# Kernel optimization log

Measured on AMD Instinct MI355X. Metric: run time of the kernel, lower is better.

The kernel has to match this reference:

```python
import jax, jax.numpy as jnp
import numpy as np

N = 512  # n_inputs = n_layers (even)


def setup_inputs() -> dict:
    key = jax.random.key(0)
    ks = jax.random.split(key, 8)
    H = N // 2
    two_pi = 2.0 * np.pi
    return {
        "thetas_full": jax.random.uniform(ks[0], (N, N), jnp.float32, 0.0, two_pi),
        "thetas_inout": jax.random.uniform(ks[1], (2, N), jnp.float32, 0.0, two_pi),
        "pc_losses_full": 0.05 * jax.random.uniform(ks[2], (N, N), jnp.float32),
        "pc_losses_inout": 0.05 * jax.random.uniform(ks[3], (2, N), jnp.float32),
        "mmi_losses_even": 0.05 * jax.random.uniform(ks[4], (N, H), jnp.float32),
        "mmi_losses_odd": 0.05 * jax.random.uniform(ks[5], (N, H - 1), jnp.float32),
        "mmi_imb_even": jax.random.uniform(ks[6], (N, H), jnp.float32, -0.05, 0.05),
        "mmi_imb_odd": jax.random.uniform(ks[7], (N, H - 1), jnp.float32, -0.05, 0.05),
    }


def _pc(M, theta, loss):
    # diag(sqrt(1-loss) * exp(i*theta)) @ M  -- phase shifter on every waveguide
    a = jnp.sqrt(1.0 - loss) * jnp.exp(1j * theta)  # complex64 [n]
    return a[:, None] * M


def _mmi_pairs(top, bot, loss, imb):
    # 2x2 MMI coupler sqrt(1-loss) * [[t, i r], [i r, t]], t=sqrt(.5+imb), r=sqrt(.5-imb)
    a = jnp.sqrt(1.0 - loss)[:, None]
    t = (a * jnp.sqrt(0.5 + imb)[:, None]).astype(top.dtype)
    r = (a * jnp.sqrt(0.5 - imb)[:, None])
    ir = (1j * r).astype(top.dtype)
    return t * top + ir * bot, ir * top + t * bot


def _mmi_even(M, loss, imb):
    # couplers on row pairs (0,1),(2,3),...
    n = M.shape[0]
    P = M.reshape(n // 2, 2, n)
    top, bot = _mmi_pairs(P[:, 0], P[:, 1], loss, imb)
    return jnp.stack([top, bot], axis=1).reshape(n, n)


def _mmi_odd(M, loss, imb):
    # couplers on row pairs (1,2),(3,4),...; rows 0 and n-1 pass through
    n = M.shape[0]
    P = M[1:-1].reshape(n // 2 - 1, 2, n)
    top, bot = _mmi_pairs(P[:, 0], P[:, 1], loss, imb)
    inner = jnp.stack([top, bot], axis=1).reshape(n - 2, n)
    return jnp.concatenate([M[:1], inner, M[-1:]], axis=0)


def _forward(thetas_full, thetas_inout, pc_losses_full, pc_losses_inout,
             mmi_losses_even, mmi_losses_odd, mmi_imb_even, mmi_imb_odd):
    n = thetas_full.shape[1]
    h = n // 2
    M = jnp.eye(n, dtype=jnp.complex64)
    M = _pc(M, thetas_inout[0], pc_losses_inout[0])
    # pack params two layers per scan step (loop body uses indices 2i and 2i+1)
    xs = (thetas_full.reshape(h, 2, n), pc_losses_full.reshape(h, 2, n),
          mmi_losses_even.reshape(h, 2, h), mmi_imb_even.reshape(h, 2, h),
          mmi_losses_odd.reshape(h, 2, h - 1), mmi_imb_odd.reshape(h, 2, h - 1))

    def step(M, x):
        th, lp, le, ie, lo, io = x
        M = _mmi_even(M, le[0], ie[0])
        M = _pc(M, th[0], lp[0])
        M = _mmi_even(M, le[1], ie[1])
        M = _mmi_odd(M, lo[0], io[0])
        M = _pc(M, th[1], lp[1])
        M = _mmi_odd(M, lo[1], io[1])
        return M, None

    M, _ = jax.lax.scan(jax.checkpoint(step), M, xs)
    return _pc(M, thetas_inout[1], pc_losses_inout[1])


def reference(thetas_full, thetas_inout, pc_losses_full, pc_losses_inout,
              mmi_losses_even, mmi_losses_odd, mmi_imb_even, mmi_imb_odd):
    return _forward(thetas_full, thetas_inout, pc_losses_full, pc_losses_inout,
                    mmi_losses_even, mmi_losses_odd, mmi_imb_even, mmi_imb_odd)
```

## Files before the change

### kernel.cpp

```cpp
#include <hip/hip_runtime.h>
#include <math.h>

#define NROWS   512
#define NSTEPS  256
#define PKSTEPS (NSTEPS + 2)

__device__ float4 g_pk[PKSTEPS * 5 * 256];
__device__ float2 g_io[1024];


__device__ __forceinline__ float2 pc_coef(float th, float loss) {
  float a = sqrtf(1.0f - loss);
  float s, c;
  sincosf(th, &s, &c);
  return make_float2(a * c, a * s);
}
__device__ __forceinline__ float2 mmi_coef(float loss, float imb) {
  float a = sqrtf(1.0f - loss);
  return make_float2(a * sqrtf(0.5f + imb), a * sqrtf(0.5f - imb));
}

__global__ void precomp_kernel(const float* __restrict__ thf,
                               const float* __restrict__ thio,
                               const float* __restrict__ lpf,
                               const float* __restrict__ lpio,
                               const float* __restrict__ le,
                               const float* __restrict__ lo,
                               const float* __restrict__ ie,
                               const float* __restrict__ io2) {
  const int b   = blockIdx.x;
  const int tid = threadIdx.x;
  if (b >= NSTEPS) {
    int j = (b - NSTEPS) * 256 + tid;
    g_io[j]       = pc_coef(thio[j],       lpio[j]);
    g_io[j + 512] = pc_coef(thio[j + 512], lpio[j + 512]);
    return;
  }
  const int i  = b;
  const int w  = tid >> 6, l = tid & 63;
  const int R0 = 128 * w + 2 * l;
  const int p  = 64 * w + l;
  const int L0 = 2 * i, L1 = 2 * i + 1;

  float2 e0  = mmi_coef(le[L0 * 256 + p], ie[L0 * 256 + p]);
  float2 e1  = mmi_coef(le[L1 * 256 + p], ie[L1 * 256 + p]);
  float2 p0a = pc_coef(thf[L0 * 512 + R0],     lpf[L0 * 512 + R0]);
  float2 p0b = pc_coef(thf[L0 * 512 + R0 + 1], lpf[L0 * 512 + R0 + 1]);
  float2 p1a = pc_coef(thf[L1 * 512 + R0],     lpf[L1 * 512 + R0]);
  float2 p1b = pc_coef(thf[L1 * 512 + R0 + 1], lpf[L1 * 512 + R0 + 1]);
  float2 one = make_float2(1.0f, 0.0f);
  float2 o0T = (p <= 254) ? mmi_coef(lo[L0 * 255 + p],     io2[L0 * 255 + p])     : one;
  float2 o0B = (p >= 1)   ? mmi_coef(lo[L0 * 255 + p - 1], io2[L0 * 255 + p - 1]) : one;
  float2 o1T = (p <= 254) ? mmi_coef(lo[L1 * 255 + p],     io2[L1 * 255 + p])     : one;
  float2 o1B = (p >= 1)   ? mmi_coef(lo[L1 * 255 + p - 1], io2[L1 * 255 + p - 1]) : one;

  float4* base = g_pk + (i * 5) * 256 + tid;
  base[0]        = make_float4(e0.x,  e0.y,  e1.x,  e1.y);
  base[256]      = make_float4(p0a.x, p0a.y, p0b.x, p0b.y);
  base[2 * 256]  = make_float4(o0T.x, o0T.y, o0B.x, o0B.y);
  base[3 * 256]  = make_float4(p1a.x, p1a.y, p1b.x, p1b.y);
  base[4 * 256]  = make_float4(o1T.x, o1T.y, o1B.x, o1B.y);
}


__device__ __forceinline__ void barrier_lgkm() {
  asm volatile("s_waitcnt lgkmcnt(0)\n\ts_barrier" ::: "memory");
  __builtin_amdgcn_sched_barrier(0);
}

__device__ __forceinline__ void cmul(float2& v, float ar, float ai) {
  float xr = ar * v.x - ai * v.y;
  float xi = ar * v.y + ai * v.x;
  v.x = xr; v.y = xi;
}
__device__ __forceinline__ void mmix(float2& top, float2& bot, float t, float r) {
  float a = t * top.x - r * bot.y;
  float b = t * top.y + r * bot.x;
  float c = t * bot.x - r * top.y;
  float d = t * bot.y + r * top.x;
  top.x = a; top.y = b; bot.x = c; bot.y = d;
}
__device__ __forceinline__ void upd(float2& v, float t, float r, float2 o) {
  float xr = t * v.x - r * o.y;
  float xi = t * v.y + r * o.x;
  v.x = xr; v.y = xi;
}

__global__ __launch_bounds__(256) void prop_kernel(float* __restrict__ out,
                                                   int write_complex) {
  __shared__ float2 sUp[2][2][4];
  __shared__ float2 sDn[2][2][4];
  const int tid = threadIdx.x;
  const int l = tid & 63, w = tid >> 6;
  const int R0 = 128 * w + 2 * l;
  const int colbase = blockIdx.x * 2;

  float2 v[2][2];
  #pragma unroll
  for (int c = 0; c < 2; ++c)
    #pragma unroll
    for (int k = 0; k < 2; ++k)
      v[c][k] = (colbase + c == R0 + k) ? make_float2(1.0f, 0.0f)
                                        : make_float2(0.0f, 0.0f);

  auto odd = [&](float4 c, int sid) {
    float2 nb0, nb1, pt0, pt1;
    nb0.x = __shfl_down(v[0][0].x, 1); nb0.y = __shfl_down(v[0][0].y, 1);
    nb1.x = __shfl_down(v[1][0].x, 1); nb1.y = __shfl_down(v[1][0].y, 1);
    pt0.x = __shfl_up(v[0][1].x, 1);   pt0.y = __shfl_up(v[0][1].y, 1);
    pt1.x = __shfl_up(v[1][1].x, 1);   pt1.y = __shfl_up(v[1][1].y, 1);
    if (l == 0)  { sDn[0][sid][w] = v[0][0]; sDn[1][sid][w] = v[1][0]; }
    if (l == 63) { sUp[0][sid][w] = v[0][1]; sUp[1][sid][w] = v[1][1]; }
    barrier_lgkm();
    if (l == 63 && w < 3) { nb0 = sDn[0][sid][w + 1]; nb1 = sDn[1][sid][w + 1]; }
    if (l == 0 && w > 0)  { pt0 = sUp[0][sid][w - 1]; pt1 = sUp[1][sid][w - 1]; }
    if (!(w == 3 && l == 63)) {
      upd(v[0][1], c.x, c.y, nb0);
      upd(v[1][1], c.x, c.y, nb1);
    }
    if (!(w == 0 && l == 0)) {
      upd(v[0][0], c.z, c.w, pt0);
      upd(v[1][0], c.z, c.w, pt1);
    }
  };

  auto step = [&](float4 f0, float4 f1, float4 f2, float4 f3, float4 f4) {
    mmix(v[0][0], v[0][1], f0.x, f0.y);
    mmix(v[1][0], v[1][1], f0.x, f0.y);
    cmul(v[0][0], f1.x, f1.y); cmul(v[1][0], f1.x, f1.y);
    cmul(v[0][1], f1.z, f1.w); cmul(v[1][1], f1.z, f1.w);
    mmix(v[0][0], v[0][1], f0.z, f0.w);
    mmix(v[1][0], v[1][1], f0.z, f0.w);
    odd(f2, 0);
    cmul(v[0][0], f3.x, f3.y); cmul(v[1][0], f3.x, f3.y);
    cmul(v[0][1], f3.z, f3.w); cmul(v[1][1], f3.z, f3.w);
    odd(f4, 1);
  };

  {
    float4 a = *(const float4*)(g_io + R0);
    cmul(v[0][0], a.x, a.y); cmul(v[1][0], a.x, a.y);
    cmul(v[0][1], a.z, a.w); cmul(v[1][1], a.z, a.w);
  }

  const float4* P = g_pk + tid;
  float4 a0 = P[0],        a1 = P[256],        a2 = P[512],
         a3 = P[768],      a4 = P[1024];
  float4 b0 = P[1280],     b1 = P[1280+256],   b2 = P[1280+512],
         b3 = P[1280+768], b4 = P[1280+1024];

  #pragma unroll 1
  for (int i = 0; i < NSTEPS; i += 2) {
    const float4* Q = P + (i + 2) * 1280;
    float4 n0 = Q[0], n1 = Q[256], n2 = Q[512], n3 = Q[768], n4 = Q[1024];
    step(a0, a1, a2, a3, a4);
    a0 = n0; a1 = n1; a2 = n2; a3 = n3; a4 = n4;
    const float4* R = P + (i + 3) * 1280;
    n0 = R[0]; n1 = R[256]; n2 = R[512]; n3 = R[768]; n4 = R[1024];
    step(b0, b1, b2, b3, b4);
    b0 = n0; b1 = n1; b2 = n2; b3 = n3; b4 = n4;
  }

  {
    float4 a = *(const float4*)(g_io + 512 + R0);
    cmul(v[0][0], a.x, a.y); cmul(v[1][0], a.x, a.y);
    cmul(v[0][1], a.z, a.w); cmul(v[1][1], a.z, a.w);
  }

  if (write_complex) {
    float2* o = (float2*)out;
    #pragma unroll
    for (int c = 0; c < 2; ++c) {
      o[(R0 + 0) * NROWS + colbase + c] = v[c][0];
      o[(R0 + 1) * NROWS + colbase + c] = v[c][1];
    }
  } else {
    #pragma unroll
    for (int c = 0; c < 2; ++c) {
      out[(R0 + 0) * NROWS + colbase + c] = v[c][0].x;
      out[(R0 + 1) * NROWS + colbase + c] = v[c][1].x;
    }
  }
}


extern "C" void kernel_launch(void* const* d_in, const int* in_sizes, int n_in,
                              void* d_out, int out_size, void* d_ws, size_t ws_size,
                              hipStream_t stream) {
  const float* thf  = (const float*)d_in[0];
  const float* thio = (const float*)d_in[1];
  const float* lpf  = (const float*)d_in[2];
  const float* lpio = (const float*)d_in[3];
  const float* le   = (const float*)d_in[4];
  const float* lo   = (const float*)d_in[5];
  const float* ie   = (const float*)d_in[6];
  const float* io2  = (const float*)d_in[7];

  const int write_complex = (out_size >= 2 * NROWS * NROWS) ? 1 : 0;

  precomp_kernel<<<NSTEPS + 2, 256, 0, stream>>>(
      thf, thio, lpf, lpio, le, lo, ie, io2);
  prop_kernel<<<NROWS / 2, 256, 0, stream>>>((float*)d_out, write_complex);
}
```

Before: 223.5 us.

## Deepen coefficient prefetch to four steps with inline-asm loads and vmcnt waits

Replaces the compiler-scheduled two-step register double buffer for per-step coefficients with a four-deep ring of hand-issued global_load_dwordx4 instructions. Before each step it waits with s_waitcnt vmcnt(15), so the three later steps' loads stay in flight. The goal is to hide global-load latency in the serial 256-step propagation loop. It costs more live VGPRs (20 float4 buffers), and the packed array grows by two padding steps so the tail prefetches stay in bounds. It also relies on fragile inline asm whose ordering the compiler cannot see.

```diff
diff --git a/kernel.cpp b/kernel.cpp
--- a/kernel.cpp
+++ b/kernel.cpp
@@ -1,9 +1,12 @@
 #include <hip/hip_runtime.h>
 #include <math.h>
+#include <stdint.h>
 
 #define NROWS   512
 #define NSTEPS  256
-#define PKSTEPS (NSTEPS + 2)
+#define PKSTEPS (NSTEPS + 4)
+#define SLOTB   4096u
+#define STEPB   20480u
 
 __device__ float4 g_pk[PKSTEPS * 5 * 256];
 __device__ float2 g_io[1024];
@@ -63,6 +66,8 @@
 }
 
 
+typedef float f4 __attribute__((ext_vector_type(4)));
+
 __device__ __forceinline__ void barrier_lgkm() {
   asm volatile("s_waitcnt lgkmcnt(0)\n\ts_barrier" ::: "memory");
   __builtin_amdgcn_sched_barrier(0);
@@ -86,8 +91,24 @@
   v.x = xr; v.y = xi;
 }
 
-__global__ __launch_bounds__(256) void prop_kernel(float* __restrict__ out,
-                                                   int write_complex) {
+#define DECLB(V) f4 V##s0, V##s1, V##s2, V##s3, V##s4
+
+#define ISSUE(V) do { \
+  asm volatile("global_load_dwordx4 %0, %1, %2" : "=v"(V##s0) : "v"(vo0), "s"(pkb)); \
+  asm volatile("global_load_dwordx4 %0, %1, %2" : "=v"(V##s1) : "v"(vo1), "s"(pkb)); \
+  asm volatile("global_load_dwordx4 %0, %1, %2" : "=v"(V##s2) : "v"(vo2), "s"(pkb)); \
+  asm volatile("global_load_dwordx4 %0, %1, %2" : "=v"(V##s3) : "v"(vo3), "s"(pkb)); \
+  asm volatile("global_load_dwordx4 %0, %1, %2" : "=v"(V##s4) : "v"(vo4), "s"(pkb)); \
+  vo0 += STEPB; vo1 += STEPB; vo2 += STEPB; vo3 += STEPB; vo4 += STEPB; \
+} while (0)
+
+#define WAITP() do { \
+  asm volatile("s_waitcnt vmcnt(15)"); \
+  __builtin_amdgcn_sched_barrier(0); \
+} while (0)
+
+__global__ __launch_bounds__(256, 1) void prop_kernel(float* __restrict__ out,
+                                                      int write_complex) {
   __shared__ float2 sUp[2][2][4];
   __shared__ float2 sDn[2][2][4];
   const int tid = threadIdx.x;
@@ -103,7 +124,7 @@
       v[c][k] = (colbase + c == R0 + k) ? make_float2(1.0f, 0.0f)
                                         : make_float2(0.0f, 0.0f);
 
-  auto odd = [&](float4 c, int sid) {
+  auto odd = [&](f4 c, int sid) {
     float2 nb0, nb1, pt0, pt1;
     nb0.x = __shfl_down(v[0][0].x, 1); nb0.y = __shfl_down(v[0][0].y, 1);
     nb1.x = __shfl_down(v[1][0].x, 1); nb1.y = __shfl_down(v[1][0].y, 1);
@@ -115,26 +136,26 @@
     if (l == 63 && w < 3) { nb0 = sDn[0][sid][w + 1]; nb1 = sDn[1][sid][w + 1]; }
     if (l == 0 && w > 0)  { pt0 = sUp[0][sid][w - 1]; pt1 = sUp[1][sid][w - 1]; }
     if (!(w == 3 && l == 63)) {
-      upd(v[0][1], c.x, c.y, nb0);
-      upd(v[1][1], c.x, c.y, nb1);
+      upd(v[0][1], c[0], c[1], nb0);
+      upd(v[1][1], c[0], c[1], nb1);
     }
     if (!(w == 0 && l == 0)) {
-      upd(v[0][0], c.z, c.w, pt0);
-      upd(v[1][0], c.z, c.w, pt1);
+      upd(v[0][0], c[2], c[3], pt0);
+      upd(v[1][0], c[2], c[3], pt1);
     }
   };
 
-  auto step = [&](float4 f0, float4 f1, float4 f2, float4 f3, float4 f4) {
-    mmix(v[0][0], v[0][1], f0.x, f0.y);
-    mmix(v[1][0], v[1][1], f0.x, f0.y);
-    cmul(v[0][0], f1.x, f1.y); cmul(v[1][0], f1.x, f1.y);
-    cmul(v[0][1], f1.z, f1.w); cmul(v[1][1], f1.z, f1.w);
-    mmix(v[0][0], v[0][1], f0.z, f0.w);
-    mmix(v[1][0], v[1][1], f0.z, f0.w);
-    odd(f2, 0);
-    cmul(v[0][0], f3.x, f3.y); cmul(v[1][0], f3.x, f3.y);
-    cmul(v[0][1], f3.z, f3.w); cmul(v[1][1], f3.z, f3.w);
-    odd(f4, 1);
+  auto step = [&](f4 q0, f4 q1, f4 q2, f4 q3, f4 q4) {
+    mmix(v[0][0], v[0][1], q0[0], q0[1]);
+    mmix(v[1][0], v[1][1], q0[0], q0[1]);
+    cmul(v[0][0], q1[0], q1[1]); cmul(v[1][0], q1[0], q1[1]);
+    cmul(v[0][1], q1[2], q1[3]); cmul(v[1][1], q1[2], q1[3]);
+    mmix(v[0][0], v[0][1], q0[2], q0[3]);
+    mmix(v[1][0], v[1][1], q0[2], q0[3]);
+    odd(q2, 0);
+    cmul(v[0][0], q3[0], q3[1]); cmul(v[1][0], q3[0], q3[1]);
+    cmul(v[0][1], q3[2], q3[3]); cmul(v[1][1], q3[2], q3[3]);
+    odd(q4, 1);
   };
 
   {
@@ -143,22 +164,23 @@
     cmul(v[0][1], a.z, a.w); cmul(v[1][1], a.z, a.w);
   }
 
-  const float4* P = g_pk + tid;
-  float4 a0 = P[0],        a1 = P[256],        a2 = P[512],
-         a3 = P[768],      a4 = P[1024];
-  float4 b0 = P[1280],     b1 = P[1280+256],   b2 = P[1280+512],
-         b3 = P[1280+768], b4 = P[1280+1024];
+  const uintptr_t pkb = (uintptr_t)(const void*)g_pk;
+  uint32_t vo0 = (uint32_t)tid * 16u;
+  uint32_t vo1 = vo0 + SLOTB, vo2 = vo0 + 2u * SLOTB,
+           vo3 = vo0 + 3u * SLOTB, vo4 = vo0 + 4u * SLOTB;
+
+  DECLB(A); DECLB(B); DECLB(C); DECLB(D);
+  ISSUE(A);
+  ISSUE(B);
+  ISSUE(C);
+  ISSUE(D);
 
   #pragma unroll 1
-  for (int i = 0; i < NSTEPS; i += 2) {
-    const float4* Q = P + (i + 2) * 1280;
-    float4 n0 = Q[0], n1 = Q[256], n2 = Q[512], n3 = Q[768], n4 = Q[1024];
-    step(a0, a1, a2, a3, a4);
-    a0 = n0; a1 = n1; a2 = n2; a3 = n3; a4 = n4;
-    const float4* R = P + (i + 3) * 1280;
-    n0 = R[0]; n1 = R[256]; n2 = R[512]; n3 = R[768]; n4 = R[1024];
-    step(b0, b1, b2, b3, b4);
-    b0 = n0; b1 = n1; b2 = n2; b3 = n3; b4 = n4;
+  for (int i = 0; i < NSTEPS; i += 4) {
+    WAITP(); step(As0, As1, As2, As3, As4); ISSUE(A);
+    WAITP(); step(Bs0, Bs1, Bs2, Bs3, Bs4); ISSUE(B);
+    WAITP(); step(Cs0, Cs1, Cs2, Cs3, Cs4); ISSUE(C);
+    WAITP(); step(Ds0, Ds1, Ds2, Ds3, Ds4); ISSUE(D);
   }
 
   {
```

After: 222.8 us. About the same (-0.3%).
